# Kernel tuning notes

Hardware: AMD Instinct MI355X
Metric: run time of the kernel (lower is better)

## Reference

```python
import jax, jax.numpy as jnp
import numpy as np

DEPTH = 4      # truncation depth of the signature
DIM = 8        # path channels
PATH_LEN = 16384
STREAM = True


def _restricted_exp(z, depth):
    # exp(z) in truncated tensor algebra: level k term = z^{\otimes k}/k!, flattened to [d**k]
    terms = [z]
    for k in range(2, depth + 1):
        terms.append((terms[-1][:, None] * z[None, :]).reshape(-1) / k)
    return tuple(terms)


def _chen_mult(a, b, depth):
    # Truncated tensor-algebra product (Chen's relation); a_0 = b_0 = 1 implicit.
    # c_k = a_k + b_k + sum_{i=1}^{k-1} a_i \otimes b_{k-i}
    c = []
    for k in range(depth):
        t = a[k] + b[k]
        for i in range(k):
            t = t + (a[i][:, None] * b[k - 1 - i][None, :]).reshape(-1)
        c.append(t)
    return tuple(c)


def setup_inputs() -> dict:
    key = jax.random.key(0)
    path = jax.random.normal(key, (PATH_LEN, DIM), dtype=jnp.float32)
    return {"path": path}


def reference(path):
    depth = DEPTH
    d = path.shape[-1]
    inc = path[1:] - path[:-1]                                # [N-1, d] increments
    exps = jax.vmap(lambda z: _restricted_exp(z, depth))(inc)  # tuple of [N-1, d**k]
    init = tuple(jnp.zeros((d ** (k + 1),), dtype=path.dtype) for k in range(depth))

    def step(carry, x):
        new = _chen_mult(carry, x, depth)
        return new, (new if STREAM else None)

    last, ys = jax.lax.scan(step, init, exps)
    if STREAM:
        # flatten: concat levels -> [N-1, d + d^2 + ... + d^depth]
        return jnp.concatenate([y for y in ys], axis=-1)
    return jnp.concatenate(last, axis=-1)
```

## Files before the change

### kernel.cpp

```cpp
#include <hip/hip_runtime.h>

#define NPATH 16384
#define DIM   8
#define NINC  (NPATH - 1)
#define SIG   4680
#define L1OFF 0
#define L2OFF 8
#define L3OFF 72
#define L4OFF 584
#define NCHUNK 256
#define CHUNK  64
#define NSUB  2048
#define SUB   8
#define NGRP  16
#define GSIZE 16
#define C6    0.16666666666666666f
#define LPAD  17


__device__ __forceinline__ void light_barrier() {
  asm volatile("s_waitcnt lgkmcnt(0)" ::: "memory");
  __builtin_amdgcn_s_barrier();
}

__device__ __forceinline__ void zero_state(float r4[16], float r3[2],
                                           float& a1i, float& a2v,
                                           float& a2s, float& a1s, float& a1t) {
#pragma unroll
  for (int l = 0; l < 16; ++l) r4[l] = 0.f;
  r3[0] = r3[1] = 0.f;
  a1i = a2v = a2s = a1s = a1t = 0.f;
}

__device__ __forceinline__ void store_sig_reg(float* dst,
                                              const float r4[16], const float r3[2],
                                              float a2s, float a1t, int t) {
  float4* d4 = (float4*)(dst + L4OFF + 16 * t);
  d4[0] = make_float4(r4[0], r4[1], r4[2], r4[3]);
  d4[1] = make_float4(r4[4], r4[5], r4[6], r4[7]);
  d4[2] = make_float4(r4[8], r4[9], r4[10], r4[11]);
  d4[3] = make_float4(r4[12], r4[13], r4[14], r4[15]);
  *(float2*)(dst + L3OFF + 2 * t) = make_float2(r3[0], r3[1]);
  if (t < 64) dst[L2OFF + t] = a2s;
  if (t < 8)  dst[L1OFF + t] = a1t;
}

__device__ __forceinline__ void load_state(const float* __restrict__ src,
                                           float r4[16], float r3[2],
                                           float& a1i, float& a2v,
                                           float& a2s, float& a1s, float& a1t, int t) {
  const float4* s4 = (const float4*)(src + L4OFF + 16 * t);
  float4 G0 = s4[0], G1 = s4[1], G2 = s4[2], G3 = s4[3];
  r4[0]=G0.x; r4[1]=G0.y; r4[2]=G0.z; r4[3]=G0.w;
  r4[4]=G1.x; r4[5]=G1.y; r4[6]=G1.z; r4[7]=G1.w;
  r4[8]=G2.x; r4[9]=G2.y; r4[10]=G2.z; r4[11]=G2.w;
  r4[12]=G3.x; r4[13]=G3.y; r4[14]=G3.z; r4[15]=G3.w;
  const float2 gr3 = *(const float2*)(src + L3OFF + 2 * t);
  r3[0] = gr3.x; r3[1] = gr3.y;
  a1i = src[L1OFF + (t >> 5)];
  a2v = src[L2OFF + (t >> 2)];
  a2s = a1s = a1t = 0.f;
  if (t < 64) { a2s = src[L2OFF + t]; a1s = src[L1OFF + (t >> 3)]; }
  if (t < 8)  { a1t = src[L1OFF + t]; }
}

__device__ __forceinline__ void chen_reg(float r4[16], float r3[2],
                                         float& a1i, float& a2v,
                                         float& a2s, float& a1s, float& a1t,
                                         const float* b, int t) {
  const int i   = t >> 5;
  const int j   = (t >> 2) & 7;
  const int ij  = t >> 2;
  const int c0  = 2 * t;
  const int jk0 = c0 & 63;
  const int k0  = 2 * (t & 3);
  const int i2  = t >> 3;
  const int j2  = t & 7;
  const float4* bv = (const float4*)b;
  float4 B0 = bv[146 + 4 * t], B1 = bv[147 + 4 * t], B2 = bv[148 + 4 * t], B3 = bv[149 + 4 * t];
  float4 Cq0 = bv[18 + 2 * jk0], Cq1 = bv[19 + 2 * jk0], Cq2 = bv[20 + 2 * jk0], Cq3 = bv[21 + 2 * jk0];
  float4 D0 = bv[2 + 2 * k0], D1 = bv[3 + 2 * k0], D2 = bv[4 + 2 * k0], D3 = bv[5 + 2 * k0];
  float4 E0 = bv[0], E1 = bv[1];
  const float2 b3c  = *(const float2*)(b + L3OFF + c0);
  const float2 b2jk = *(const float2*)(b + L2OFF + jk0);
  const float2 b1k  = *(const float2*)(b + L1OFF + k0);
  const float b2ij = b[L2OFF + ij];
  const float b1j  = b[L1OFF + j];
  const float b1i  = b[L1OFF + i];
  float b2t = 0.f, b1j2 = 0.f, b1i2 = 0.f, b1t = 0.f;
  if (t < 64) { b2t = b[L2OFF + t]; b1j2 = b[L1OFF + j2]; b1i2 = b[L1OFF + i2]; }
  if (t < 8)  { b1t = b[L1OFF + t]; }

  const float b4r[16] = {B0.x,B0.y,B0.z,B0.w, B1.x,B1.y,B1.z,B1.w,
                         B2.x,B2.y,B2.z,B2.w, B3.x,B3.y,B3.z,B3.w};
  const float b3r[16] = {Cq0.x,Cq0.y,Cq0.z,Cq0.w, Cq1.x,Cq1.y,Cq1.z,Cq1.w,
                         Cq2.x,Cq2.y,Cq2.z,Cq2.w, Cq3.x,Cq3.y,Cq3.z,Cq3.w};
  const float b2r[16] = {D0.x,D0.y,D0.z,D0.w, D1.x,D1.y,D1.z,D1.w,
                         D2.x,D2.y,D2.z,D2.w, D3.x,D3.y,D3.z,D3.w};
  const float b1r[8]  = {E0.x,E0.y,E0.z,E0.w, E1.x,E1.y,E1.z,E1.w};

#pragma unroll
  for (int l = 0; l < 8; ++l) {
    r4[l]     += b4r[l]     + a1i * b3r[l]     + a2v * b2r[l]     + r3[0] * b1r[l];
    r4[8 + l] += b4r[8 + l] + a1i * b3r[8 + l] + a2v * b2r[8 + l] + r3[1] * b1r[l];
  }
  r3[0] += b3c.x + a1i * b2jk.x + a2v * b1k.x;
  r3[1] += b3c.y + a1i * b2jk.y + a2v * b1k.y;
  const float a1i_old = a1i;
  a2v += b2ij + a1i_old * b1j;
  if (t < 64) { a2s += b2t + a1s * b1j2; a1s += b1i2; }
  a1i = a1i_old + b1i;
  if (t < 8) a1t += b1t;
}

__device__ __forceinline__ void step_update(const float* zs,
                                            float r4[16], float r3[2],
                                            float& a1i, float& a2v,
                                            float& a2s, float& a1s, float& a1t, int t) {
  const int i  = t >> 5;
  const int j  = (t >> 2) & 7;
  const int k0 = 2 * (t & 3);
  const int i2 = t >> 3;
  const int j2 = t & 7;
  const float zi = zs[i];
  const float zj = zs[j];
  const float2 zk = *(const float2*)(zs + k0);
  const float4 za = *(const float4*)zs;
  const float4 zb = *(const float4*)(zs + 4);
  const float zn[8] = {za.x, za.y, za.z, za.w, zb.x, zb.y, zb.z, zb.w};
  const float a1zi4 = a1i + 0.25f * zi;
  const float zj6   = C6 * zj;
  const float T0 = r3[0] + a2v * (0.5f * zk.x) + a1zi4 * (zj6 * zk.x);
  const float T1 = r3[1] + a2v * (0.5f * zk.y) + a1zi4 * (zj6 * zk.y);
  const float U  = a2v + (0.5f * a1i + C6 * zi) * zj;
#pragma unroll
  for (int l = 0; l < 8; ++l) {
    r4[l]     += T0 * zn[l];
    r4[8 + l] += T1 * zn[l];
  }
  r3[0] += zk.x * U;
  r3[1] += zk.y * U;
  a2v += (a1i + 0.5f * zi) * zj;
  a1i += zi;
  if (t < 64) {
    const float zi2 = zs[i2], zj2v = zs[j2];
    a2s += (a1s + 0.5f * zi2) * zj2v;
    a1s += zi2;
  }
  if (t < 8) a1t += zs[t];
}

__global__ __launch_bounds__(256) void k_totals(const float* __restrict__ path,
                                                float* __restrict__ T64,
                                                float* __restrict__ snap) {
  __shared__ float zbuf[CHUNK][8];
  const int t = threadIdx.x;
  const int b = blockIdx.x;
  const int base = b * CHUNK;
  for (int u = t; u < CHUNK * 8; u += 256) {
    const int s = u >> 3, l = u & 7;
    const int rB = min(base + s + 1, NPATH - 1);
    zbuf[s][l] = path[rB * DIM + l] - path[(base + s) * DIM + l];
  }
  float r4[16], r3[2], a1i, a2v, a2s, a1s, a1t;
  zero_state(r4, r3, a1i, a2v, a2s, a1s, a1t);
  __syncthreads();
  for (int w = 0; w < 8; ++w) {
    store_sig_reg(snap + ((size_t)b * 8 + w) * SIG, r4, r3, a2s, a1t, t);
#pragma unroll
    for (int s2 = 0; s2 < 8; ++s2)
      step_update(zbuf[8 * w + s2], r4, r3, a1i, a2v, a2s, a1s, a1t, t);
  }
  store_sig_reg(T64 + (size_t)b * SIG, r4, r3, a2s, a1t, t);
}

__global__ __launch_bounds__(256) void k_scan(const float* __restrict__ in,
                                              float* __restrict__ prefout,
                                              float* __restrict__ totout,
                                              int count) {
  const int t = threadIdx.x;
  const size_t goff = (size_t)blockIdx.x * count;
  float r4[16], r3[2], a1i, a2v, a2s, a1s, a1t;
  zero_state(r4, r3, a1i, a2v, a2s, a1s, a1t);
  for (int m = 0; m < count; ++m) {
    store_sig_reg(prefout + (goff + m) * SIG, r4, r3, a2s, a1t, t);
    chen_reg(r4, r3, a1i, a2v, a2s, a1s, a1t, in + (goff + m) * SIG, t);
  }
  if (totout != nullptr) store_sig_reg(totout + (size_t)blockIdx.x * SIG, r4, r3, a2s, a1t, t);
}

__global__ __launch_bounds__(256) void k_out(const float* __restrict__ path,
                                             const float* __restrict__ pref,
                                             const float* __restrict__ gpref,
                                             const float* __restrict__ snap,
                                             float* __restrict__ out) {
  __shared__ float zbuf[SUB][8];
  __shared__ __align__(16) float lbuf[256 * LPAD];
  const int t = threadIdx.x;
  const int sIdx = blockIdx.x;
  const int b = sIdx >> 3;
  const int g = b >> 4;
  const int base = sIdx * SUB;
  const int n = min(SUB, NINC - base);
  if (t < SUB * 8) {
    const int s = t >> 3, l = t & 7;
    const int rB = min(base + s + 1, NPATH - 1);
    zbuf[s][l] = path[rB * DIM + l] - path[(base + s) * DIM + l];
  }
  float r4[16], r3[2], a1i, a2v, a2s, a1s, a1t;
  load_state(gpref + (size_t)g * SIG, r4, r3, a1i, a2v, a2s, a1s, a1t, t);
  chen_reg(r4, r3, a1i, a2v, a2s, a1s, a1t, pref + (size_t)b * SIG, t);
  chen_reg(r4, r3, a1i, a2v, a2s, a1s, a1t, snap + (size_t)sIdx * SIG, t);
  __syncthreads();
  const int tp = t >> 2;
  const int rq = 4 * (t & 3);
  for (int s2 = 0; s2 < n; ++s2) {
    step_update(zbuf[s2], r4, r3, a1i, a2v, a2s, a1s, a1t, t);
    float* lb = lbuf + LPAD * t;
    *(float4*)(lb + 0)  = make_float4(r4[0], r4[1], r4[2], r4[3]);
    *(float4*)(lb + 4)  = make_float4(r4[4], r4[5], r4[6], r4[7]);
    *(float4*)(lb + 8)  = make_float4(r4[8], r4[9], r4[10], r4[11]);
    *(float4*)(lb + 12) = make_float4(r4[12], r4[13], r4[14], r4[15]);
    light_barrier();
    float* dst = out + (size_t)(base + s2) * SIG;
#pragma unroll
    for (int q = 0; q < 4; ++q) {
      const float4 v = *(const float4*)(lbuf + LPAD * (tp + 64 * q) + rq);
      *(float4*)(dst + L4OFF + 4 * t + 1024 * q) = v;
    }
    *(float2*)(dst + L3OFF + 2 * t) = make_float2(r3[0], r3[1]);
    if (t < 64) dst[L2OFF + t] = a2s;
    if (t < 8)  dst[L1OFF + t] = a1t;
    light_barrier();
  }
}

extern "C" void kernel_launch(void* const* d_in, const int* in_sizes, int n_in,
                              void* d_out, int out_size, void* d_ws, size_t ws_size,
                              hipStream_t stream) {
  (void)in_sizes; (void)n_in; (void)out_size; (void)ws_size;
  const float* path = (const float*)d_in[0];
  float* out = (float*)d_out;
  float* ws = (float*)d_ws;

  float* T64   = ws;
  float* pref  = T64   + (size_t)NCHUNK * SIG;
  float* gtot  = pref  + (size_t)NCHUNK * SIG;
  float* gpref = gtot  + (size_t)NGRP * SIG;
  float* snap  = gpref + (size_t)NGRP * SIG;

  k_totals<<<NCHUNK, 256, 0, stream>>>(path, T64, snap);
  k_scan<<<NGRP, 256, 0, stream>>>(T64, pref, gtot, GSIZE);
  k_scan<<<1, 256, 0, stream>>>(gtot, gpref, nullptr, NGRP);
  k_out<<<NSUB, 256, 0, stream>>>(path, pref, gpref, snap, out);
}
```

Before: 141.0 us.

## Prefetch scan operands, split state combine into separate kernel, raise stream occupancy

```diff
diff --git a/kernel.cpp b/kernel.cpp
--- a/kernel.cpp
+++ b/kernel.cpp
@@ -32,7 +32,7 @@
   a1i = a2v = a2s = a1s = a1t = 0.f;
 }
 
-__device__ __forceinline__ void store_sig_reg(float* dst,
+__device__ __forceinline__ void store_sig_reg(float* __restrict__ dst,
                                               const float r4[16], const float r3[2],
                                               float a2s, float a1t, int t) {
   float4* d4 = (float4*)(dst + L4OFF + 16 * t);
@@ -64,10 +64,16 @@
   if (t < 8)  { a1t = src[L1OFF + t]; }
 }
 
-__device__ __forceinline__ void chen_reg(float r4[16], float r3[2],
-                                         float& a1i, float& a2v,
-                                         float& a2s, float& a1s, float& a1t,
-                                         const float* b, int t) {
+struct ChenB {
+  float4 B0, B1, B2, B3;
+  float4 C0, C1, C2, C3;
+  float4 D0, D1, D2, D3;
+  float4 E0, E1;
+  float2 b3c, b2jk, b1k;
+  float  b2ij, b1j, b1i, b2t, b1j2, b1i2, b1t;
+};
+
+__device__ __forceinline__ void chen_load(const float* __restrict__ b, int t, ChenB& R) {
   const int i   = t >> 5;
   const int j   = (t >> 2) & 7;
   const int ij  = t >> 2;
@@ -77,40 +83,44 @@
   const int i2  = t >> 3;
   const int j2  = t & 7;
   const float4* bv = (const float4*)b;
-  float4 B0 = bv[146 + 4 * t], B1 = bv[147 + 4 * t], B2 = bv[148 + 4 * t], B3 = bv[149 + 4 * t];
-  float4 Cq0 = bv[18 + 2 * jk0], Cq1 = bv[19 + 2 * jk0], Cq2 = bv[20 + 2 * jk0], Cq3 = bv[21 + 2 * jk0];
-  float4 D0 = bv[2 + 2 * k0], D1 = bv[3 + 2 * k0], D2 = bv[4 + 2 * k0], D3 = bv[5 + 2 * k0];
-  float4 E0 = bv[0], E1 = bv[1];
-  const float2 b3c  = *(const float2*)(b + L3OFF + c0);
-  const float2 b2jk = *(const float2*)(b + L2OFF + jk0);
-  const float2 b1k  = *(const float2*)(b + L1OFF + k0);
-  const float b2ij = b[L2OFF + ij];
-  const float b1j  = b[L1OFF + j];
-  const float b1i  = b[L1OFF + i];
-  float b2t = 0.f, b1j2 = 0.f, b1i2 = 0.f, b1t = 0.f;
-  if (t < 64) { b2t = b[L2OFF + t]; b1j2 = b[L1OFF + j2]; b1i2 = b[L1OFF + i2]; }
-  if (t < 8)  { b1t = b[L1OFF + t]; }
-
-  const float b4r[16] = {B0.x,B0.y,B0.z,B0.w, B1.x,B1.y,B1.z,B1.w,
-                         B2.x,B2.y,B2.z,B2.w, B3.x,B3.y,B3.z,B3.w};
-  const float b3r[16] = {Cq0.x,Cq0.y,Cq0.z,Cq0.w, Cq1.x,Cq1.y,Cq1.z,Cq1.w,
-                         Cq2.x,Cq2.y,Cq2.z,Cq2.w, Cq3.x,Cq3.y,Cq3.z,Cq3.w};
-  const float b2r[16] = {D0.x,D0.y,D0.z,D0.w, D1.x,D1.y,D1.z,D1.w,
-                         D2.x,D2.y,D2.z,D2.w, D3.x,D3.y,D3.z,D3.w};
-  const float b1r[8]  = {E0.x,E0.y,E0.z,E0.w, E1.x,E1.y,E1.z,E1.w};
-
+  R.B0 = bv[146 + 4 * t]; R.B1 = bv[147 + 4 * t]; R.B2 = bv[148 + 4 * t]; R.B3 = bv[149 + 4 * t];
+  R.C0 = bv[18 + 2 * jk0]; R.C1 = bv[19 + 2 * jk0]; R.C2 = bv[20 + 2 * jk0]; R.C3 = bv[21 + 2 * jk0];
+  R.D0 = bv[2 + 2 * k0]; R.D1 = bv[3 + 2 * k0]; R.D2 = bv[4 + 2 * k0]; R.D3 = bv[5 + 2 * k0];
+  R.E0 = bv[0]; R.E1 = bv[1];
+  R.b3c  = *(const float2*)(b + L3OFF + c0);
+  R.b2jk = *(const float2*)(b + L2OFF + jk0);
+  R.b1k  = *(const float2*)(b + L1OFF + k0);
+  R.b2ij = b[L2OFF + ij];
+  R.b1j  = b[L1OFF + j];
+  R.b1i  = b[L1OFF + i];
+  R.b2t = 0.f; R.b1j2 = 0.f; R.b1i2 = 0.f; R.b1t = 0.f;
+  if (t < 64) { R.b2t = b[L2OFF + t]; R.b1j2 = b[L1OFF + j2]; R.b1i2 = b[L1OFF + i2]; }
+  if (t < 8)  { R.b1t = b[L1OFF + t]; }
+}
+
+__device__ __forceinline__ void chen_apply(float r4[16], float r3[2],
+                                           float& a1i, float& a2v,
+                                           float& a2s, float& a1s, float& a1t,
+                                           const ChenB& R, int t) {
+  const float b4r[16] = {R.B0.x,R.B0.y,R.B0.z,R.B0.w, R.B1.x,R.B1.y,R.B1.z,R.B1.w,
+                         R.B2.x,R.B2.y,R.B2.z,R.B2.w, R.B3.x,R.B3.y,R.B3.z,R.B3.w};
+  const float b3r[16] = {R.C0.x,R.C0.y,R.C0.z,R.C0.w, R.C1.x,R.C1.y,R.C1.z,R.C1.w,
+                         R.C2.x,R.C2.y,R.C2.z,R.C2.w, R.C3.x,R.C3.y,R.C3.z,R.C3.w};
+  const float b2r[16] = {R.D0.x,R.D0.y,R.D0.z,R.D0.w, R.D1.x,R.D1.y,R.D1.z,R.D1.w,
+                         R.D2.x,R.D2.y,R.D2.z,R.D2.w, R.D3.x,R.D3.y,R.D3.z,R.D3.w};
+  const float b1r[8]  = {R.E0.x,R.E0.y,R.E0.z,R.E0.w, R.E1.x,R.E1.y,R.E1.z,R.E1.w};
 #pragma unroll
   for (int l = 0; l < 8; ++l) {
     r4[l]     += b4r[l]     + a1i * b3r[l]     + a2v * b2r[l]     + r3[0] * b1r[l];
     r4[8 + l] += b4r[8 + l] + a1i * b3r[8 + l] + a2v * b2r[8 + l] + r3[1] * b1r[l];
   }
-  r3[0] += b3c.x + a1i * b2jk.x + a2v * b1k.x;
-  r3[1] += b3c.y + a1i * b2jk.y + a2v * b1k.y;
+  r3[0] += R.b3c.x + a1i * R.b2jk.x + a2v * R.b1k.x;
+  r3[1] += R.b3c.y + a1i * R.b2jk.y + a2v * R.b1k.y;
   const float a1i_old = a1i;
-  a2v += b2ij + a1i_old * b1j;
-  if (t < 64) { a2s += b2t + a1s * b1j2; a1s += b1i2; }
-  a1i = a1i_old + b1i;
-  if (t < 8) a1t += b1t;
+  a2v += R.b2ij + a1i_old * R.b1j;
+  if (t < 64) { a2s += R.b2t + a1s * R.b1j2; a1s += R.b1i2; }
+  a1i = a1i_old + R.b1i;
+  if (t < 8) a1t += R.b1t;
 }
 
 __device__ __forceinline__ void step_update(const float* zs,
@@ -182,24 +192,45 @@
   const size_t goff = (size_t)blockIdx.x * count;
   float r4[16], r3[2], a1i, a2v, a2s, a1s, a1t;
   zero_state(r4, r3, a1i, a2v, a2s, a1s, a1t);
-  for (int m = 0; m < count; ++m) {
+  ChenB bA, bB;
+  chen_load(in + goff * SIG, t, bA);
+  for (int m = 0; m < count; m += 2) {
+    if (m + 1 < count) chen_load(in + (goff + m + 1) * SIG, t, bB);
     store_sig_reg(prefout + (goff + m) * SIG, r4, r3, a2s, a1t, t);
-    chen_reg(r4, r3, a1i, a2v, a2s, a1s, a1t, in + (goff + m) * SIG, t);
+    chen_apply(r4, r3, a1i, a2v, a2s, a1s, a1t, bA, t);
+    if (m + 1 >= count) break;
+    if (m + 2 < count) chen_load(in + (goff + m + 2) * SIG, t, bA);
+    store_sig_reg(prefout + (goff + m + 1) * SIG, r4, r3, a2s, a1t, t);
+    chen_apply(r4, r3, a1i, a2v, a2s, a1s, a1t, bB, t);
   }
   if (totout != nullptr) store_sig_reg(totout + (size_t)blockIdx.x * SIG, r4, r3, a2s, a1t, t);
 }
 
-__global__ __launch_bounds__(256) void k_out(const float* __restrict__ path,
-                                             const float* __restrict__ pref,
-                                             const float* __restrict__ gpref,
-                                             const float* __restrict__ snap,
-                                             float* __restrict__ out) {
-  __shared__ float zbuf[SUB][8];
-  __shared__ __align__(16) float lbuf[256 * LPAD];
+__global__ __launch_bounds__(256) void k_states(const float* __restrict__ pref,
+                                                const float* __restrict__ gpref,
+                                                const float* __restrict__ snap,
+                                                float* __restrict__ states) {
   const int t = threadIdx.x;
   const int sIdx = blockIdx.x;
   const int b = sIdx >> 3;
   const int g = b >> 4;
+  float r4[16], r3[2], a1i, a2v, a2s, a1s, a1t;
+  ChenB cA, cB;
+  chen_load(pref + (size_t)b * SIG, t, cA);
+  chen_load(snap + (size_t)sIdx * SIG, t, cB);
+  load_state(gpref + (size_t)g * SIG, r4, r3, a1i, a2v, a2s, a1s, a1t, t);
+  chen_apply(r4, r3, a1i, a2v, a2s, a1s, a1t, cA, t);
+  chen_apply(r4, r3, a1i, a2v, a2s, a1s, a1t, cB, t);
+  store_sig_reg(states + (size_t)sIdx * SIG, r4, r3, a2s, a1t, t);
+}
+
+__global__ __launch_bounds__(256, 8) void k_stream(const float* __restrict__ path,
+                                                   const float* __restrict__ states,
+                                                   float* __restrict__ out) {
+  __shared__ float zbuf[SUB][8];
+  __shared__ __align__(16) float lbuf[256 * LPAD];
+  const int t = threadIdx.x;
+  const int sIdx = blockIdx.x;
   const int base = sIdx * SUB;
   const int n = min(SUB, NINC - base);
   if (t < SUB * 8) {
@@ -208,9 +239,7 @@
     zbuf[s][l] = path[rB * DIM + l] - path[(base + s) * DIM + l];
   }
   float r4[16], r3[2], a1i, a2v, a2s, a1s, a1t;
-  load_state(gpref + (size_t)g * SIG, r4, r3, a1i, a2v, a2s, a1s, a1t, t);
-  chen_reg(r4, r3, a1i, a2v, a2s, a1s, a1t, pref + (size_t)b * SIG, t);
-  chen_reg(r4, r3, a1i, a2v, a2s, a1s, a1t, snap + (size_t)sIdx * SIG, t);
+  load_state(states + (size_t)sIdx * SIG, r4, r3, a1i, a2v, a2s, a1s, a1t, t);
   __syncthreads();
   const int tp = t >> 2;
   const int rq = 4 * (t & 3);
@@ -243,14 +272,16 @@
   float* out = (float*)d_out;
   float* ws = (float*)d_ws;
 
-  float* T64   = ws;
-  float* pref  = T64   + (size_t)NCHUNK * SIG;
-  float* gtot  = pref  + (size_t)NCHUNK * SIG;
-  float* gpref = gtot  + (size_t)NGRP * SIG;
-  float* snap  = gpref + (size_t)NGRP * SIG;
+  float* T64    = ws;
+  float* pref   = T64    + (size_t)NCHUNK * SIG;
+  float* gtot   = pref   + (size_t)NCHUNK * SIG;
+  float* gpref  = gtot   + (size_t)NGRP * SIG;
+  float* snap   = gpref  + (size_t)NGRP * SIG;
+  float* states = snap   + (size_t)NSUB * SIG;
 
   k_totals<<<NCHUNK, 256, 0, stream>>>(path, T64, snap);
   k_scan<<<NGRP, 256, 0, stream>>>(T64, pref, gtot, GSIZE);
   k_scan<<<1, 256, 0, stream>>>(gtot, gpref, nullptr, NGRP);
-  k_out<<<NSUB, 256, 0, stream>>>(path, pref, gpref, snap, out);
-}
+  k_states<<<NSUB, 256, 0, stream>>>(pref, gpref, snap, states);
+  k_stream<<<NSUB, 256, 0, stream>>>(path, states, out);
+}
```

Measured after the change: 165.5 us. 1.17x slower.
